# Performance work log

Hardware: AMD Instinct MI355X
Metric: run time of the kernel (lower is better)

The kernel has to match this reference:

```python
import jax, jax.numpy as jnp
import numpy as np

N_ENT = 100000
N_USR = 30000
N_TOT = N_ENT + N_USR
N_REL = 32
D = 64
E = 500000
INTER = 500000
N_LAYERS = 2
SLOPE = 0.01  # torch nn.LeakyReLU default negative slope


def _seg_softmax(logits, seg, n):
    # sparse softmax over rows (segments)
    m = jax.ops.segment_max(logits, seg, num_segments=n)
    ex = jnp.exp(logits - m[seg])
    den = jax.ops.segment_sum(ex, seg, num_segments=n)
    return ex / den[seg]


def setup_inputs() -> dict:
    key = jax.random.key(0)
    k = jax.random.split(key, 14)
    all_embed = jax.random.normal(k[0], (N_TOT, D), jnp.float32) * 0.1
    rel_embed = jax.random.normal(k[1], (N_REL, D), jnp.float32) * 0.1
    Wk_w = jax.random.normal(k[2], (D, 2 * D), jnp.float32) / np.sqrt(2 * D)
    Wk_b = jnp.zeros((D,), jnp.float32)
    Wa_w = jax.random.normal(k[3], (D, D), jnp.float32) / np.sqrt(D)
    Wb_w = jax.random.normal(k[4], (D, D), jnp.float32) / np.sqrt(D)
    # KG edge lists (head entity, tail entity, relation)
    h_list = jnp.sort(jax.random.randint(k[5], (E,), 0, N_ENT))
    t_list = jax.random.randint(k[6], (E,), 0, N_ENT)
    r_list = jax.random.randint(k[7], (E,), 0, N_REL)
    # bipartite interaction matrix A_in (symmetric, items rows first then users)
    u = jax.random.randint(k[8], (INTER,), 0, N_USR)
    it = jax.random.randint(k[9], (INTER,), 0, N_ENT)
    a_row = jnp.concatenate([it, N_ENT + u])
    a_col = jnp.concatenate([N_ENT + u, it])
    a_vals = jax.random.uniform(k[10], (2 * INTER,), jnp.float32) * 0.01
    # calc_score ids: user ids are offset by n_entities in the concatenated table
    user_ids = N_ENT + jax.random.randint(k[11], (1024,), 0, N_USR)
    item_ids = jax.random.randint(k[12], (2048,), 0, N_ENT)
    return dict(all_embed=all_embed, rel_embed=rel_embed, Wk_w=Wk_w, Wk_b=Wk_b,
                Wa_w=Wa_w, Wb_w=Wb_w, a_vals=a_vals, user_ids=user_ids,
                item_ids=item_ids, h_list=h_list, t_list=t_list, r_list=r_list,
                a_row=a_row, a_col=a_col)


def _get_embeddings(all_embed, rel_embed, Wk_w, Wk_b, Wa_w, Wb_w, a_vals,
                    h_list, t_list, r_list, a_row, a_col):
    e_ent = all_embed[:N_ENT]
    e_usr = all_embed[N_ENT:]
    user_list = [e_usr]
    item_list = [e_ent]
    e_items_dual = e_ent
    e_users_curr = e_usr
    e_ent_curr = e_ent
    r_e = rel_embed[r_list]  # (E, D) -- constant across layers
    for _ in range(N_LAYERS):
        # --- KG attention (Eq. 2): gather + concat + linear + dot + leakyrelu ---
        h_e = e_ent_curr[h_list]            # (E, D)
        t_e = e_ent_curr[t_list]            # (E, D)
        cat = jnp.concatenate([t_e, h_e], axis=1)   # (E, 2D)
        trans = cat @ Wk_w.T + Wk_b                 # (E, D)
        logits = jnp.sum(trans * r_e, axis=1)       # (E,)
        vals = jnp.where(logits >= 0, logits, SLOPE * logits)
        alpha = _seg_softmax(vals, h_list, N_ENT)   # row-wise sparse softmax
        # --- KG aggregation (Eq. 1): spmm ---
        e_items_kg = jax.ops.segment_sum(alpha[:, None] * t_e, h_list,
                                         num_segments=N_ENT)
        # --- IG aggregation (Eq. 3 & 6): spmm with A_in ---
        ig_in = jnp.concatenate([e_items_dual, e_users_curr], axis=0)  # (N_TOT, D)
        ig_out = jax.ops.segment_sum(a_vals[:, None] * ig_in[a_col], a_row,
                                     num_segments=N_TOT)
        e_items_collab = ig_out[:N_ENT]
        e_users_new = ig_out[N_ENT:]
        # --- fusion gate (Eq. 4, 5) ---
        g = jax.nn.sigmoid(e_items_kg @ Wa_w.T + e_items_collab @ Wb_w.T)
        e_items_dual = g * e_items_kg + (1.0 - g) * e_items_collab
        item_list.append(e_items_collab)
        user_list.append(e_users_new)
        e_users_curr = e_users_new
        e_ent_curr = e_items_kg
    item_final = sum(item_list)
    user_final = sum(user_list)
    return jnp.concatenate([item_final, user_final], axis=0)


def reference(all_embed, rel_embed, Wk_w, Wk_b, Wa_w, Wb_w, a_vals,
              user_ids, item_ids, h_list, t_list, r_list, a_row, a_col):
    all_final = _get_embeddings(all_embed, rel_embed, Wk_w, Wk_b, Wa_w, Wb_w,
                                a_vals, h_list, t_list, r_list, a_row, a_col)
    user_e = all_final[user_ids]   # (Bu, D)
    item_e = all_final[item_ids]   # (Bi, D)
    return user_e @ item_e.T       # (Bu, Bi)
```

## Files before the change

### kernel.cpp

```cpp
#include <hip/hip_runtime.h>
#include <hip/hip_bf16.h>

#define N_ENT 100000
#define N_USR 30000
#define N_TOTN 130000
#define N_RELC 32
#define DIM 64
#define NEDGE 500000
#define INTER 500000
#define SLOPE 0.01f
#define CPT_NB 127
#define FILL_NB 1954
#define ATT_NB 1024
#define RSTR 64

typedef unsigned char u8;
typedef unsigned long long u64;

__device__ __forceinline__ float grp_sum16(float v){
  v += __shfl_xor(v, 8, 64);
  v += __shfl_xor(v, 4, 64);
  v += __shfl_xor(v, 2, 64);
  v += __shfl_xor(v, 1, 64);
  return v;
}

__global__ void __launch_bounds__(256) k_prep(
    const float* __restrict__ rel, const float* __restrict__ Wk,
    const float* __restrict__ Wkb, float* __restrict__ m, float* __restrict__ b,
    const int* __restrict__ user_ids, const int* __restrict__ item_ids,
    u8* __restrict__ r2_item, u8* __restrict__ r2_user){
  int bid = blockIdx.x;
  if (bid < 17){
    int idx = bid*256 + threadIdx.x;
    if (idx < N_RELC*128){
      int r = idx >> 7, j = idx & 127;
      float s = 0.f;
      for (int d = 0; d < DIM; ++d) s += rel[r*DIM+d] * Wk[d*128+j];
      m[idx] = s;
    } else if (idx < N_RELC*128 + N_RELC){
      int r = idx - N_RELC*128;
      float s = 0.f;
      for (int d = 0; d < DIM; ++d) s += Wkb[d] * rel[r*DIM+d];
      b[r] = s;
    }
  } else {
    int i = (bid - 17)*256 + threadIdx.x;
    if (i < 1024) r2_user[user_ids[i] - N_ENT] = 1;
    else if (i < 3072) r2_item[item_ids[i - 1024]] = 1;
  }
}

__global__ void k_mark(const int* __restrict__ a_row, const int* __restrict__ a_col,
                       const u8* __restrict__ r2_item, const u8* __restrict__ r2_user,
                       u8* __restrict__ need_d, u8* __restrict__ need_u){
  int i = blockIdx.x*256 + threadIdx.x;
  if (i >= INTER) return;
  int it = a_row[i];
  int uu = a_col[i] - N_ENT;
  if (r2_item[it]) need_u[uu] = 1;
  if (r2_user[uu]) need_d[it] = 1;
}

__global__ void __launch_bounds__(256) k_buildfill(
    const int* __restrict__ a_row, const int* __restrict__ a_col,
    const float* __restrict__ a_vals,
    const u8* __restrict__ need_d, const u8* __restrict__ need_u,
    const u8* __restrict__ r2_item, const u8* __restrict__ r2_user,
    int* __restrict__ list_gate, int* __restrict__ list_s1,
    int* __restrict__ counters, int* __restrict__ cnt, int2* __restrict__ csr){
  if (blockIdx.x < CPT_NB){
    __shared__ u64 mg_sh[16], ms_sh[16];
    __shared__ int pre_g[16], pre_s[16];
    __shared__ int base_sh[2];
    int t = threadIdx.x;
    int wave = t >> 6, lane = t & 63;
    bool pg[4], ps[4];
    int ibase = blockIdx.x*1024;
    #pragma unroll
    for (int k = 0; k < 4; ++k){
      int i = ibase + k*256 + t;
      bool g = false, s = false;
      if (i < N_TOTN){
        if (i < N_ENT){ g = need_d[i] != 0; s = g || (r2_item[i] != 0); }
        else { int u = i - N_ENT; s = (need_u[u] != 0) || (r2_user[u] != 0); }
      }
      pg[k] = g; ps[k] = s;
      u64 mg = __ballot(g), ms = __ballot(s);
      if (lane == 0){ mg_sh[k*4 + wave] = mg; ms_sh[k*4 + wave] = ms; }
    }
    __syncthreads();
    if (t == 0){
      int sg = 0, ss = 0;
      for (int j = 0; j < 16; ++j){
        pre_g[j] = sg; sg += __popcll(mg_sh[j]);
        pre_s[j] = ss; ss += __popcll(ms_sh[j]);
      }
      base_sh[0] = sg ? atomicAdd(&counters[0], sg) : 0;
      base_sh[1] = ss ? atomicAdd(&counters[1], ss) : 0;
    }
    __syncthreads();
    int bg = base_sh[0], bs = base_sh[1];
    u64 lmask = (1ull << lane) - 1;
    #pragma unroll
    for (int k = 0; k < 4; ++k){
      int i = ibase + k*256 + t;
      if (pg[k]) list_gate[bg + pre_g[k*4+wave] + __popcll(mg_sh[k*4+wave] & lmask)] = i;
      if (ps[k]) list_s1 [bs + pre_s[k*4+wave] + __popcll(ms_sh[k*4+wave] & lmask)] = i;
    }
  } else {
    int i = (blockIdx.x - CPT_NB)*256 + threadIdx.x;
    if (i >= INTER) return;
    int it = a_row[i];
    int uc = a_col[i];
    int uu = uc - N_ENT;
    if (need_d[it] | r2_item[it]){
      int p = atomicAdd(&cnt[it], 1);
      if (p < RSTR) csr[((size_t)it << 6) + p] = make_int2(uc, __float_as_int(a_vals[i]));
    }
    if (need_u[uu] | r2_user[uu]){
      int p = atomicAdd(&cnt[uc], 1);
      if (p < RSTR) csr[((size_t)uc << 6) + p] = make_int2(it, __float_as_int(a_vals[i + INTER]));
    }
  }
}

__global__ void __launch_bounds__(256) k_l1(const float4* __restrict__ ent4,
    const float4* __restrict__ m4, const float* __restrict__ bvec,
    const int* __restrict__ h_list, const int* __restrict__ t_list,
    const int* __restrict__ r_list, const int* __restrict__ list_gate,
    const int* __restrict__ list_s1, const int* __restrict__ counters,
    float4* __restrict__ kg4, const int* __restrict__ cnt,
    const int2* __restrict__ csr,
    float4* __restrict__ collab4, float4* __restrict__ x2_4){
  if (blockIdx.x < ATT_NB){
    __shared__ float4 msh[N_RELC*32];
    __shared__ float bsh[N_RELC];
    for (int i = threadIdx.x; i < N_RELC*32; i += 256) msh[i] = m4[i];
    if (threadIdx.x < N_RELC) bsh[threadIdx.x] = bvec[threadIdx.x];
    __syncthreads();
    int n = counters[0];
    int sub = threadIdx.x & 15;
    int grp = (blockIdx.x*256 + threadIdx.x) >> 4;
    int ng = (ATT_NB*256) >> 4;
    for (int idx = grp; idx < n; idx += ng){
      int s = list_gate[idx];
      int lo = 0, hi = NEDGE;
      while (lo < hi){ int mid = (lo + hi) >> 1; if (h_list[mid] < s) lo = mid + 1; else hi = mid; }
      int beg = lo;
      hi = NEDGE;
      while (lo < hi){ int mid = (lo + hi) >> 1; if (h_list[mid] <= s) lo = mid + 1; else hi = mid; }
      int end = lo;
      float4 h4 = ent4[(size_t)s*16 + sub];
      float l = 0.f;
      float4 acc = {0.f,0.f,0.f,0.f};
      for (int base = beg; base < end; base += 16){
        int mch = end - base; if (mch > 16) mch = 16;
        int tj = 0, rj = 0;
        if (sub < mch){ tj = t_list[base + sub]; rj = r_list[base + sub]; }
        #pragma unroll 4
        for (int j = 0; j < mch; ++j){
          int ti = __shfl(tj, j, 16);
          int r  = __shfl(rj, j, 16);
          float4 t4 = ent4[(size_t)ti*16 + sub];
          float4 mt = msh[r*32 + sub];
          float4 mh = msh[r*32 + 16 + sub];
          float v = t4.x*mt.x + t4.y*mt.y + t4.z*mt.z + t4.w*mt.w
                  + h4.x*mh.x + h4.y*mh.y + h4.z*mh.z + h4.w*mh.w;
          v = grp_sum16(v) + bsh[r];
          v = (v >= 0.f) ? v : SLOPE * v;
          float w = __expf(v);
          l += w;
          acc.x += w*t4.x; acc.y += w*t4.y; acc.z += w*t4.z; acc.w += w*t4.w;
        }
      }
      float inv = (end > beg) ? 1.f / l : 0.f;
      float4 o = {acc.x*inv, acc.y*inv, acc.z*inv, acc.w*inv};
      kg4[(size_t)s*16 + sub] = o;
    }
  } else {
    int n = counters[1];
    int sub = threadIdx.x & 15;
    int bid = blockIdx.x - ATT_NB;
    int nb = gridDim.x - ATT_NB;
    int grp = (bid*256 + threadIdx.x) >> 4;
    int ng = (nb*256) >> 4;
    for (int idx = grp; idx < n; idx += ng){
      int i = list_s1[idx];
      int deg = cnt[i]; if (deg > RSTR) deg = RSTR;
      size_t base0 = (size_t)i << 6;
      float4 acc = {0.f,0.f,0.f,0.f};
      for (int b = 0; b < deg; b += 16){
        int mch = deg - b; if (mch > 16) mch = 16;
        int2 e = make_int2(0, 0);
        if (sub < mch) e = csr[base0 + b + sub];
        #pragma unroll 4
        for (int j = 0; j < mch; ++j){
          int cj = __shfl(e.x, j, 16);
          float vj = __int_as_float(__shfl(e.y, j, 16));
          float4 sv = ent4[(size_t)cj*16 + sub];
          acc.x += vj*sv.x; acc.y += vj*sv.y; acc.z += vj*sv.z; acc.w += vj*sv.w;
        }
      }
      if (i < N_ENT) collab4[(size_t)i*16 + sub] = acc;
      else x2_4[(size_t)i*16 + sub] = acc;
    }
  }
}

__global__ void __launch_bounds__(256) k_gate(const float* __restrict__ kg,
    const float* __restrict__ collab, const float* __restrict__ Wa,
    const float* __restrict__ Wb, float* __restrict__ x2dual,
    const int* __restrict__ list, const int* __restrict__ counters){
  int n = counters[0];
  int row0 = blockIdx.x * 64;
  if (row0 >= n) return;
  __shared__ float Xsh[64][129];
  __shared__ float Wsh[128][65];
  for (int i = threadIdx.x; i < 64*64; i += 256){
    int a = i >> 6, j = i & 63;
    Wsh[j][a] = Wa[i];
    Wsh[64 + j][a] = Wb[i];
  }
  for (int i = threadIdx.x; i < 64*128; i += 256){
    int r = i >> 7, c = i & 127;
    int idx = row0 + r;
    float v = 0.f;
    if (idx < n){
      int row = list[idx];
      v = (c < 64) ? kg[(size_t)row*64 + c] : collab[(size_t)row*64 + (c - 64)];
    }
    Xsh[r][c] = v;
  }
  __syncthreads();
  int ct = threadIdx.x & 15, rt = threadIdx.x >> 4;
  int r0 = rt * 4, c0 = ct * 4;
  float acc[4][4] = {};
  for (int k = 0; k < 128; ++k){
    float w0 = Wsh[k][c0], w1 = Wsh[k][c0+1], w2 = Wsh[k][c0+2], w3 = Wsh[k][c0+3];
    #pragma unroll
    for (int i = 0; i < 4; ++i){
      float x = Xsh[r0+i][k];
      acc[i][0] += x*w0; acc[i][1] += x*w1; acc[i][2] += x*w2; acc[i][3] += x*w3;
    }
  }
  #pragma unroll
  for (int i = 0; i < 4; ++i){
    int idx = row0 + r0 + i;
    if (idx < n){
      int row = list[idx];
      float4 o;
      #pragma unroll
      for (int j = 0; j < 4; ++j){
        int c = c0 + j;
        float g = 1.f / (1.f + __expf(-acc[i][j]));
        float kv = Xsh[r0+i][c];
        float cv = Xsh[r0+i][64 + c];
        (&o.x)[j] = g*kv + (1.f - g)*cv;
      }
      *(float4*)&x2dual[(size_t)row*64 + c0] = o;
    }
  }
}

__global__ void __launch_bounds__(256) k_spmm2g(const int* __restrict__ cnt,
    const int2* __restrict__ csr, const float* __restrict__ x2,
    const float* __restrict__ all_embed, const float* __restrict__ collab1,
    const int* __restrict__ user_ids, const int* __restrict__ item_ids,
    float* __restrict__ user_e, float* __restrict__ item_e){
  int lane = threadIdx.x & 63;
  int g = (blockIdx.x*256 + threadIdx.x) >> 6;
  if (g >= 3072) return;
  int id;
  float b1;
  if (g < 1024){
    id = user_ids[g];
    b1 = x2[(size_t)id*64 + lane];
  } else {
    id = item_ids[g - 1024];
    b1 = collab1[(size_t)id*64 + lane];
  }
  float acc = all_embed[(size_t)id*64 + lane] + b1;
  int deg = cnt[id]; if (deg > RSTR) deg = RSTR;
  size_t base0 = (size_t)id << 6;
  int2 e = make_int2(0, 0);
  if (lane < deg) e = csr[base0 + lane];
  for (int j = 0; j < deg; ++j){
    int cj = __shfl(e.x, j, 64);
    float vj = __int_as_float(__shfl(e.y, j, 64));
    acc += vj * x2[(size_t)cj*64 + lane];
  }
  if (g < 1024) user_e[(size_t)g*64 + lane] = acc;
  else item_e[(size_t)(g - 1024)*64 + lane] = acc;
}

__global__ void __launch_bounds__(256) k_out(const float* __restrict__ ue,
    const float* __restrict__ ie, float* __restrict__ out){
  __shared__ float ash[32][65];
  __shared__ float bsh[32][65];
  int row0 = blockIdx.y * 32, col0 = blockIdx.x * 32;
  for (int i = threadIdx.x; i < 32*64; i += 256){
    int r = i >> 6, c = i & 63;
    ash[r][c] = ue[(size_t)(row0 + r)*DIM + c];
    bsh[r][c] = ie[(size_t)(col0 + r)*DIM + c];
  }
  __syncthreads();
  int tx = threadIdx.x & 15, ty = threadIdx.x >> 4;
  int r0 = ty*2, c0 = tx*2;
  float a00=0.f, a01=0.f, a10=0.f, a11=0.f;
  #pragma unroll
  for (int k = 0; k < 64; ++k){
    float x0 = ash[r0][k], x1 = ash[r0+1][k];
    float y0 = bsh[c0][k], y1 = bsh[c0+1][k];
    a00 += x0*y0; a01 += x0*y1; a10 += x1*y0; a11 += x1*y1;
  }
  float2 o0 = {a00, a01}, o1 = {a10, a11};
  *(float2*)&out[(size_t)(row0 + r0)*2048 + col0 + c0] = o0;
  *(float2*)&out[(size_t)(row0 + r0 + 1)*2048 + col0 + c0] = o1;
}

extern "C" void kernel_launch(void* const* d_in, const int* in_sizes, int n_in,
                              void* d_out, int out_size, void* d_ws, size_t ws_size,
                              hipStream_t stream){
  const float* all_embed = (const float*)d_in[0];
  const float* rel_embed = (const float*)d_in[1];
  const float* Wk_w      = (const float*)d_in[2];
  const float* Wk_b      = (const float*)d_in[3];
  const float* Wa_w      = (const float*)d_in[4];
  const float* Wb_w      = (const float*)d_in[5];
  const float* a_vals    = (const float*)d_in[6];
  const int* user_ids   = (const int*)d_in[7];
  const int* item_ids   = (const int*)d_in[8];
  const int* h_list     = (const int*)d_in[9];
  const int* t_list     = (const int*)d_in[10];
  const int* r_list     = (const int*)d_in[11];
  const int* a_row      = (const int*)d_in[12];
  const int* a_col      = (const int*)d_in[13];
  float* out = (float*)d_out;

  char* p = (char*)d_ws;
  auto alloc = [&](size_t bytes)->void*{
    void* r = (void*)p;
    p += (bytes + 255) & ~(size_t)255;
    return r;
  };
  float* m_rel   = (float*)alloc((size_t)N_RELC*128*4);
  float* b_rel   = (float*)alloc((size_t)N_RELC*4);
  size_t zbytes = (size_t)N_TOTN*4 + 256 + (2*(size_t)N_ENT + 2*(size_t)N_USR);
  char*  zbase  = (char*)alloc(zbytes);
  int*   cnt      = (int*)zbase;
  int*   counters = (int*)(zbase + (size_t)N_TOTN*4);
  u8*    r2_item  = (u8*)(zbase + (size_t)N_TOTN*4 + 256);
  u8*    r2_user  = r2_item + N_ENT;
  u8*    need_d   = r2_user + N_USR;
  u8*    need_u   = need_d + N_ENT;
  int2*  csr     = (int2*) alloc((size_t)N_TOTN*RSTR*8);
  int*   list_gate = (int*)alloc((size_t)N_ENT*4);
  int*   list_s1   = (int*)alloc((size_t)N_TOTN*4);
  float* kg1     = (float*)alloc((size_t)N_ENT*DIM*4);
  float* collab1 = (float*)alloc((size_t)N_ENT*DIM*4);
  float* x2      = (float*)alloc((size_t)N_TOTN*DIM*4);
  float* user_e  = (float*)alloc((size_t)1024*DIM*4);
  float* item_e  = (float*)alloc((size_t)2048*DIM*4);

  hipMemsetAsync(zbase, 0, zbytes, stream);
  k_prep<<<29, 256, 0, stream>>>(rel_embed, Wk_w, Wk_b, m_rel, b_rel,
      user_ids, item_ids, r2_item, r2_user);
  k_mark<<<(INTER + 255)/256, 256, 0, stream>>>(a_row, a_col, r2_item, r2_user, need_d, need_u);
  k_buildfill<<<CPT_NB + FILL_NB, 256, 0, stream>>>(a_row, a_col, a_vals,
      need_d, need_u, r2_item, r2_user, list_gate, list_s1, counters, cnt, csr);

  k_l1<<<ATT_NB + 2048, 256, 0, stream>>>((const float4*)all_embed,
      (const float4*)m_rel, b_rel, h_list, t_list, r_list, list_gate, list_s1,
      counters, (float4*)kg1, cnt, csr, (float4*)collab1, (float4*)x2);
  k_gate<<<(N_ENT + 63)/64, 256, 0, stream>>>(kg1, collab1, Wa_w, Wb_w, x2,
      list_gate, counters);
  k_spmm2g<<<768, 256, 0, stream>>>(cnt, csr, x2, all_embed, collab1,
      user_ids, item_ids, user_e, item_e);
  dim3 grid_out(2048/32, 1024/32);
  k_out<<<grid_out, 256, 0, stream>>>(user_e, item_e, out);
}
```

Baseline: 210.4 us.

## Build full CSR unconditionally and derive needed-node lists from query neighbors

Drops the separate marking pass over all interactions. The CSR is now filled for every node without filtering, and a new pass walks the CSR rows of the queried users and items to flag their neighbors and append them to the work lists with atomic exchange and wave-level compaction. The memset is folded into the prep kernel as float4 zero stores. This cuts one full pass over the interaction arrays and a launch, but the fill now issues twice as many unconditional atomics and CSR writes, and the list order is no longer sorted by node id.

```diff
diff --git a/kernel.cpp b/kernel.cpp
--- a/kernel.cpp
+++ b/kernel.cpp
@@ -9,10 +9,11 @@
 #define NEDGE 500000
 #define INTER 500000
 #define SLOPE 0.01f
-#define CPT_NB 127
 #define FILL_NB 1954
 #define ATT_NB 1024
 #define RSTR 64
+#define ZB16 90016
+#define ZERO_NB 352
 
 typedef unsigned char u8;
 typedef unsigned long long u64;
@@ -28,8 +29,7 @@
 __global__ void __launch_bounds__(256) k_prep(
     const float* __restrict__ rel, const float* __restrict__ Wk,
     const float* __restrict__ Wkb, float* __restrict__ m, float* __restrict__ b,
-    const int* __restrict__ user_ids, const int* __restrict__ item_ids,
-    u8* __restrict__ r2_item, u8* __restrict__ r2_user){
+    float4* __restrict__ zbase){
   int bid = blockIdx.x;
   if (bid < 17){
     int idx = bid*256 + threadIdx.x;
@@ -46,81 +46,70 @@
     }
   } else {
     int i = (bid - 17)*256 + threadIdx.x;
-    if (i < 1024) r2_user[user_ids[i] - N_ENT] = 1;
-    else if (i < 3072) r2_item[item_ids[i - 1024]] = 1;
-  }
-}
-
-__global__ void k_mark(const int* __restrict__ a_row, const int* __restrict__ a_col,
-                       const u8* __restrict__ r2_item, const u8* __restrict__ r2_user,
-                       u8* __restrict__ need_d, u8* __restrict__ need_u){
+    if (i < ZB16) zbase[i] = make_float4(0.f, 0.f, 0.f, 0.f);
+  }
+}
+
+__global__ void k_fillall(const int* __restrict__ a_row, const int* __restrict__ a_col,
+                          const float* __restrict__ a_vals,
+                          int* __restrict__ cnt, int2* __restrict__ csr){
   int i = blockIdx.x*256 + threadIdx.x;
   if (i >= INTER) return;
   int it = a_row[i];
-  int uu = a_col[i] - N_ENT;
-  if (r2_item[it]) need_u[uu] = 1;
-  if (r2_user[uu]) need_d[it] = 1;
-}
-
-__global__ void __launch_bounds__(256) k_buildfill(
-    const int* __restrict__ a_row, const int* __restrict__ a_col,
-    const float* __restrict__ a_vals,
-    const u8* __restrict__ need_d, const u8* __restrict__ need_u,
-    const u8* __restrict__ r2_item, const u8* __restrict__ r2_user,
-    int* __restrict__ list_gate, int* __restrict__ list_s1,
-    int* __restrict__ counters, int* __restrict__ cnt, int2* __restrict__ csr){
-  if (blockIdx.x < CPT_NB){
-    __shared__ u64 mg_sh[16], ms_sh[16];
-    __shared__ int pre_g[16], pre_s[16];
-    __shared__ int base_sh[2];
-    int t = threadIdx.x;
-    int wave = t >> 6, lane = t & 63;
-    bool pg[4], ps[4];
-    int ibase = blockIdx.x*1024;
-    #pragma unroll
-    for (int k = 0; k < 4; ++k){
-      int i = ibase + k*256 + t;
-      bool g = false, s = false;
-      if (i < N_TOTN){
-        if (i < N_ENT){ g = need_d[i] != 0; s = g || (r2_item[i] != 0); }
-        else { int u = i - N_ENT; s = (need_u[u] != 0) || (r2_user[u] != 0); }
+  int uc = a_col[i];
+  int p = atomicAdd(&cnt[it], 1);
+  if (p < RSTR) csr[((size_t)it << 6) + p] = make_int2(uc, __float_as_int(a_vals[i]));
+  int q = atomicAdd(&cnt[uc], 1);
+  if (q < RSTR) csr[((size_t)uc << 6) + q] = make_int2(it, __float_as_int(a_vals[i + INTER]));
+}
+
+__global__ void __launch_bounds__(256) k_mark2(
+    const int* __restrict__ user_ids, const int* __restrict__ item_ids,
+    const int* __restrict__ cnt, const int2* __restrict__ csr,
+    int* __restrict__ flag_s1, int* __restrict__ flag_g,
+    int* __restrict__ list_s1, int* __restrict__ list_gate,
+    int* __restrict__ counters){
+  int lane = threadIdx.x & 63;
+  u64 lmask = (1ull << lane) - 1;
+  if (blockIdx.x < 768){
+    int w = (blockIdx.x*256 + threadIdx.x) >> 6;
+    int id = (w < 1024) ? user_ids[w] : item_ids[w - 1024];
+    int deg = cnt[id]; if (deg > RSTR) deg = RSTR;
+    int c = -1;
+    if (lane < deg) c = csr[((size_t)id << 6) + lane].x;
+    bool ns1 = false, ng = false;
+    if (c >= 0){
+      ns1 = (atomicExch(&flag_s1[c], 1) == 0);
+      if (c < N_ENT) ng = (atomicExch(&flag_g[c], 1) == 0);
+    }
+    u64 m1 = __ballot(ns1);
+    if (m1){
+      int leader = __ffsll(m1) - 1;
+      int base = 0;
+      if (lane == leader) base = atomicAdd(&counters[1], __popcll(m1));
+      base = __shfl(base, leader, 64);
+      if (ns1) list_s1[base + __popcll(m1 & lmask)] = c;
+    }
+    u64 m2 = __ballot(ng);
+    if (m2){
+      int leader = __ffsll(m2) - 1;
+      int base = 0;
+      if (lane == leader) base = atomicAdd(&counters[0], __popcll(m2));
+      base = __shfl(base, leader, 64);
+      if (ng) list_gate[base + __popcll(m2 & lmask)] = c;
+    }
+  } else {
+    for (int i = threadIdx.x; i < 3072; i += 256){
+      int id = (i < 1024) ? user_ids[i] : item_ids[i - 1024];
+      bool ns1 = (atomicExch(&flag_s1[id], 1) == 0);
+      u64 m1 = __ballot(ns1);
+      if (m1){
+        int leader = __ffsll(m1) - 1;
+        int base = 0;
+        if (lane == leader) base = atomicAdd(&counters[1], __popcll(m1));
+        base = __shfl(base, leader, 64);
+        if (ns1) list_s1[base + __popcll(m1 & lmask)] = id;
       }
-      pg[k] = g; ps[k] = s;
-      u64 mg = __ballot(g), ms = __ballot(s);
-      if (lane == 0){ mg_sh[k*4 + wave] = mg; ms_sh[k*4 + wave] = ms; }
-    }
-    __syncthreads();
-    if (t == 0){
-      int sg = 0, ss = 0;
-      for (int j = 0; j < 16; ++j){
-        pre_g[j] = sg; sg += __popcll(mg_sh[j]);
-        pre_s[j] = ss; ss += __popcll(ms_sh[j]);
-      }
-      base_sh[0] = sg ? atomicAdd(&counters[0], sg) : 0;
-      base_sh[1] = ss ? atomicAdd(&counters[1], ss) : 0;
-    }
-    __syncthreads();
-    int bg = base_sh[0], bs = base_sh[1];
-    u64 lmask = (1ull << lane) - 1;
-    #pragma unroll
-    for (int k = 0; k < 4; ++k){
-      int i = ibase + k*256 + t;
-      if (pg[k]) list_gate[bg + pre_g[k*4+wave] + __popcll(mg_sh[k*4+wave] & lmask)] = i;
-      if (ps[k]) list_s1 [bs + pre_s[k*4+wave] + __popcll(ms_sh[k*4+wave] & lmask)] = i;
-    }
-  } else {
-    int i = (blockIdx.x - CPT_NB)*256 + threadIdx.x;
-    if (i >= INTER) return;
-    int it = a_row[i];
-    int uc = a_col[i];
-    int uu = uc - N_ENT;
-    if (need_d[it] | r2_item[it]){
-      int p = atomicAdd(&cnt[it], 1);
-      if (p < RSTR) csr[((size_t)it << 6) + p] = make_int2(uc, __float_as_int(a_vals[i]));
-    }
-    if (need_u[uu] | r2_user[uu]){
-      int p = atomicAdd(&cnt[uc], 1);
-      if (p < RSTR) csr[((size_t)uc << 6) + p] = make_int2(it, __float_as_int(a_vals[i + INTER]));
     }
   }
 }
@@ -346,14 +335,11 @@
   };
   float* m_rel   = (float*)alloc((size_t)N_RELC*128*4);
   float* b_rel   = (float*)alloc((size_t)N_RELC*4);
-  size_t zbytes = (size_t)N_TOTN*4 + 256 + (2*(size_t)N_ENT + 2*(size_t)N_USR);
-  char*  zbase  = (char*)alloc(zbytes);
+  char*  zbase    = (char*)alloc((size_t)ZB16*16);
   int*   cnt      = (int*)zbase;
   int*   counters = (int*)(zbase + (size_t)N_TOTN*4);
-  u8*    r2_item  = (u8*)(zbase + (size_t)N_TOTN*4 + 256);
-  u8*    r2_user  = r2_item + N_ENT;
-  u8*    need_d   = r2_user + N_USR;
-  u8*    need_u   = need_d + N_ENT;
+  int*   flag_s1  = (int*)(zbase + (size_t)N_TOTN*4 + 256);
+  int*   flag_g   = flag_s1 + N_TOTN;
   int2*  csr     = (int2*) alloc((size_t)N_TOTN*RSTR*8);
   int*   list_gate = (int*)alloc((size_t)N_ENT*4);
   int*   list_s1   = (int*)alloc((size_t)N_TOTN*4);
@@ -363,13 +349,11 @@
   float* user_e  = (float*)alloc((size_t)1024*DIM*4);
   float* item_e  = (float*)alloc((size_t)2048*DIM*4);
 
-  hipMemsetAsync(zbase, 0, zbytes, stream);
-  k_prep<<<29, 256, 0, stream>>>(rel_embed, Wk_w, Wk_b, m_rel, b_rel,
-      user_ids, item_ids, r2_item, r2_user);
-  k_mark<<<(INTER + 255)/256, 256, 0, stream>>>(a_row, a_col, r2_item, r2_user, need_d, need_u);
-  k_buildfill<<<CPT_NB + FILL_NB, 256, 0, stream>>>(a_row, a_col, a_vals,
-      need_d, need_u, r2_item, r2_user, list_gate, list_s1, counters, cnt, csr);
-
+  k_prep<<<17 + ZERO_NB, 256, 0, stream>>>(rel_embed, Wk_w, Wk_b, m_rel, b_rel,
+      (float4*)zbase);
+  k_fillall<<<FILL_NB, 256, 0, stream>>>(a_row, a_col, a_vals, cnt, csr);
+  k_mark2<<<769, 256, 0, stream>>>(user_ids, item_ids, cnt, csr,
+      flag_s1, flag_g, list_s1, list_gate, counters);
   k_l1<<<ATT_NB + 2048, 256, 0, stream>>>((const float4*)all_embed,
       (const float4*)m_rel, b_rel, h_list, t_list, r_list, list_gate, list_s1,
       counters, (float4*)kg1, cnt, csr, (float4*)collab1, (float4*)x2);
```

Result: slower. 304.5 us (+44.7%).
